# Performance work log

Hardware: AMD Instinct MI355X
Metric: run time of the kernel (lower is better)

Reference implementation:

```python
import jax, jax.numpy as jnp
import numpy as np
import math

D_MODEL = 1024
D_ATTN = 128
D_MID = 128
L = 4096

def setup_inputs() -> dict:
    key = jax.random.key(0)
    ks = jax.random.split(key, 5)
    scale = 1.0 / math.sqrt(D_MODEL)
    return {
        "x": jax.random.normal(ks[0], (L, D_MODEL), jnp.float32),
        "z": jax.random.normal(ks[1], (L, D_MODEL), jnp.float32),
        "Wq": jax.random.normal(ks[2], (D_MODEL, D_ATTN), jnp.float32) * scale,
        "bq": jnp.zeros((D_ATTN,), jnp.float32),
        "Wk": jax.random.normal(ks[3], (D_MODEL, D_ATTN), jnp.float32) * scale,
        "bk": jnp.zeros((D_ATTN,), jnp.float32),
        "Wv": jax.random.normal(ks[4], (D_MODEL, D_MID), jnp.float32) * scale,
        "bv": jnp.zeros((D_MID,), jnp.float32),
    }

def reference(x, z, Wq, bq, Wk, bk, Wv, bv):
    # q: [L_x, d_attn], k: [L_z, d_attn], v: [L_z, d_mid]
    q = x @ Wq + bq
    k = z @ Wk + bk
    v = z @ Wv + bv
    inv_sqrt_d = 1.0 / math.sqrt(D_ATTN)
    s = (q @ k.T) * inv_sqrt_d            # [L_x, L_z]
    y = jax.nn.softmax(s, axis=-1) @ v    # [L_x, d_mid]
    return y
```

## Files before the change

### kernel.cpp

```cpp
#include <hip/hip_runtime.h>
#include <hip/hip_bf16.h>

typedef __attribute__((ext_vector_type(8))) short short8;
typedef __attribute__((ext_vector_type(4))) float f32x4;
typedef __attribute__((ext_vector_type(8))) _Float16 half8;

#define L_SEQ 4096
#define DM    1024
#define DA    128
#define AZ    16

#define OFF_QB  786432
#define OFF_KF  1835008
#define OFF_VF  2883584
#define OFF_OA  4063232
#define OA_BYTES ((size_t)AZ * L_SEQ * DA * 2)

__device__ __forceinline__ short f2bf(float f) {
    union { float f; unsigned u; } v; v.f = f;
    unsigned u = v.u;
    u += 0x7FFFu + ((u >> 16) & 1u);
    return (short)(u >> 16);
}

__device__ __forceinline__ unsigned cvt_pk_bf16(float lo, float hi) {
    unsigned r;
    asm("v_cvt_pk_bf16_f32 %0, %1, %2" : "=v"(r) : "v"(lo), "v"(hi));
    return r;
}

typedef const __attribute__((address_space(1))) void g_void_t;
typedef __attribute__((address_space(3))) void l_void_t;
__device__ __forceinline__ void g2lds16(const void* g, void* l) {
    __builtin_amdgcn_global_load_lds((g_void_t*)g, (l_void_t*)l, 16, 0, 0);
}

__global__ __launch_bounds__(256) void prep_w_kernel(
    const float* __restrict__ Wq, const float* __restrict__ Wk,
    const float* __restrict__ Wv, short8* __restrict__ WTf)
{
    const int m = blockIdx.y, kidx = blockIdx.x;
    const float* __restrict__ W = (m == 0) ? Wq : (m == 1) ? Wk : Wv;
    __shared__ __align__(16) float Ws[32 * 132];
    const int t = threadIdx.x;
#pragma unroll
    for (int i = 0; i < 4; i++) {
        const int u = i * 256 + t;
        const int kk = u >> 5, n4 = (u & 31) * 4;
        *(f32x4*)&Ws[kk * 132 + n4] = *(const f32x4*)&W[(size_t)(kidx * 32 + kk) * DA + n4];
    }
    __syncthreads();
#pragma unroll
    for (int i = 0; i < 2; i++) {
        const int u = i * 256 + t;
        const int nt = u >> 6, lane = u & 63, l16 = lane & 15, quad = lane >> 4;
        short8 fr;
#pragma unroll
        for (int j = 0; j < 8; j++)
            fr[j] = f2bf(Ws[(quad * 8 + j) * 132 + nt * 16 + l16]);
        WTf[((size_t)(m * 32 + kidx) * 8 + nt) * 64 + lane] = fr;
    }
}

__global__ __launch_bounds__(256, 1) void qkv_kernel(
    const float* __restrict__ x, const float* __restrict__ z,
    const char* __restrict__ WTraw,
    const float* __restrict__ bq, const float* __restrict__ bk,
    const float* __restrict__ bv,
    short* __restrict__ qb, short8* __restrict__ kf, short8* __restrict__ vf)
{
    __shared__ __align__(16) char smem[2][32768];

    const int t = threadIdx.x;
    const int wave = t >> 6, lane = t & 63;
    const int l16 = lane & 15, quad = lane >> 4;
    const int mtile = wave >> 1, nhalf = wave & 1;
    const int isKV = blockIdx.y;
    const int m1 = isKV ? 1 : 0;
    const int row0 = blockIdx.x * 32;
    const int nbytes = isKV ? 32768 : 16384;

    const float* __restrict__ Am = isKV ? z : x;
    const float* ap = Am + (size_t)(row0 + mtile * 16 + l16) * DM + quad * 8;

    f32x4 acc1[4], acc2[4];
#pragma unroll
    for (int i = 0; i < 4; i++) {
        acc1[i] = (f32x4){0.f, 0.f, 0.f, 0.f};
        acc2[i] = (f32x4){0.f, 0.f, 0.f, 0.f};
    }

    auto stage = [&](int it2, int b) {
        const char* base1 = WTraw + (size_t)(m1 * 32 + it2 * 2) * 8192;
        const char* base2 = WTraw + (size_t)(2 * 32 + it2 * 2) * 8192;
#pragma unroll
        for (int i = 0; i < 8; i++) {
            const int off = i * 4096 + wave * 1024;
            if (off < nbytes) {
                const char* src = (off < 16384) ? (base1 + off) : (base2 + (off - 16384));
                g2lds16(src + lane * 16, &smem[b][off]);
            }
        }
    };

    f32x4 cur[4], nxt[4];
#pragma unroll
    for (int j = 0; j < 2; j++) {
        cur[j * 2]     = *(const f32x4*)(ap + j * 32);
        cur[j * 2 + 1] = *(const f32x4*)(ap + j * 32 + 4);
        nxt[j * 2]     = *(const f32x4*)(ap + 64 + j * 32);
        nxt[j * 2 + 1] = *(const f32x4*)(ap + 64 + j * 32 + 4);
    }

    stage(0, 0);
    __syncthreads();

#pragma unroll 1
    for (int it = 0; it < 16; it++) {
        const int b = it & 1;
        if (it + 1 < 16) stage(it + 1, b ^ 1);

        const int ipf = (it + 2 < 16) ? it + 2 : it;
        f32x4 fut[4];
#pragma unroll
        for (int j = 0; j < 2; j++) {
            fut[j * 2]     = *(const f32x4*)(ap + ipf * 64 + j * 32);
            fut[j * 2 + 1] = *(const f32x4*)(ap + ipf * 64 + j * 32 + 4);
        }

#pragma unroll
        for (int ss = 0; ss < 2; ss++) {
            short8 afr;
#pragma unroll
            for (int j = 0; j < 4; j++) {
                afr[j]     = f2bf(cur[ss * 2][j]);
                afr[4 + j] = f2bf(cur[ss * 2 + 1][j]);
            }
#pragma unroll
            for (int ntl = 0; ntl < 4; ntl++) {
                short8 bfr = *(const short8*)&smem[b][ss * 8192 + ((nhalf * 4 + ntl) * 64 + lane) * 16];
                acc1[ntl] = __builtin_amdgcn_mfma_f32_16x16x32_bf16(afr, bfr, acc1[ntl], 0, 0, 0);
            }
            if (isKV) {
#pragma unroll
                for (int ntl = 0; ntl < 4; ntl++) {
                    short8 bfr = *(const short8*)&smem[b][16384 + ss * 8192 + ((nhalf * 4 + ntl) * 64 + lane) * 16];
                    acc2[ntl] = __builtin_amdgcn_mfma_f32_16x16x32_bf16(afr, bfr, acc2[ntl], 0, 0, 0);
                }
            }
        }
        __syncthreads();
#pragma unroll
        for (int j = 0; j < 4; j++) { cur[j] = nxt[j]; nxt[j] = fut[j]; }
    }

    if (!isKV) {
        const float CL2E = 0.1275187669712930f;
#pragma unroll
        for (int ntl = 0; ntl < 4; ntl++) {
            const int col = nhalf * 64 + ntl * 16 + l16;
            const float bb = bq[col];
#pragma unroll
            for (int r = 0; r < 4; r++)
                qb[(size_t)(row0 + mtile * 16 + quad * 4 + r) * DA + col] =
                    f2bf((acc1[ntl][r] + bb) * CL2E);
        }
        return;
    }

    short* kT = (short*)&smem[0][0];
    short* vT = (short*)&smem[0][16384];
#pragma unroll
    for (int ntl = 0; ntl < 4; ntl++) {
        const int col = nhalf * 64 + ntl * 16 + l16;
        const float bbk = bk[col], bbv = bv[col];
#pragma unroll
        for (int r = 0; r < 4; r++) {
            const int rl = mtile * 16 + quad * 4 + r;
            kT[rl * 132 + col] = f2bf(acc1[ntl][r] + bbk);
            vT[rl * 132 + col] = f2bf(acc2[ntl][r] + bbv);
        }
    }
    __syncthreads();

    const int kg = blockIdx.x;
#pragma unroll
    for (int i = 0; i < 2; i++) {
        const int f = i * 256 + t;
        const int ks = f >> 7, nth = (f >> 6) & 1, ln = f & 63;
        const int lf = ln & 15, qf = ln >> 4;
        short8 fr;
#pragma unroll
        for (int j = 0; j < 8; j++)
            fr[j] = kT[(nth * 16 + lf) * 132 + ks * 32 + qf * 8 + j];
        kf[((size_t)(kg * 4 + ks) * 2 + nth) * 64 + ln] = fr;
    }
#pragma unroll
    for (int i = 0; i < 2; i++) {
        const int f = i * 256 + t;
        const int nt = f >> 6, ln = f & 63;
        const int lf = ln & 15, qf = ln >> 4;
        short8 fr;
#pragma unroll
        for (int j = 0; j < 8; j++)
            fr[j] = vT[(qf * 8 + j) * 132 + nt * 16 + lf];
        vf[((size_t)kg * 8 + nt) * 64 + ln] = fr;
    }
}

__global__ __launch_bounds__(256, 2) void attn_kernel(
    const short* __restrict__ qb, const char* __restrict__ kfg,
    const char* __restrict__ vfg, _Float16* __restrict__ OA,
    float* __restrict__ lA)
{
    __shared__ __align__(16) char kv[2][8192];

    const int t    = threadIdx.x;
    const int wave = t >> 6;
    const int lane = t & 63;
    const int l16  = lane & 15;
    const int quad = lane >> 4;
    const int qr0  = blockIdx.x * 128;
    const int g0   = blockIdx.y * 8;

    auto stage = [&](int g, int b) {
        const char* kb_ = kfg + (size_t)(g0 + g) * 8192 + wave * 2048;
        g2lds16(kb_ + lane * 16,        &kv[b][wave * 2048]);
        g2lds16(kb_ + 1024 + lane * 16, &kv[b][wave * 2048 + 1024]);
    };

    stage(0, 0);

    short8 af[2][4];
#pragma unroll
    for (int mt = 0; mt < 2; mt++) {
        const short* qrow = qb + (size_t)(qr0 + wave * 32 + mt * 16 + l16) * DA + quad * 8;
#pragma unroll
        for (int ks = 0; ks < 4; ks++)
            af[mt][ks] = *(const short8*)(qrow + ks * 32);
    }

    short8 bones;
#pragma unroll
    for (int j = 0; j < 8; j++) bones[j] = (l16 == 0) ? (short)0x3F80 : (short)0;

    f32x4 O[2][9];
#pragma unroll
    for (int mt = 0; mt < 2; mt++)
#pragma unroll
        for (int i = 0; i < 9; i++) O[mt][i] = (f32x4){0.f, 0.f, 0.f, 0.f};

    __syncthreads();

#pragma unroll 1
    for (int g = 0; g < 8; g++) {
        const int b = g & 1;
        if (g + 1 < 8) stage(g + 1, b ^ 1);

        const short8* vgp = (const short8*)(vfg + (size_t)(g0 + g) * 8192);
        short8 b2v[8];
#pragma unroll
        for (int nt = 0; nt < 8; nt++)
            b2v[nt] = vgp[nt * 64 + lane];

        const char* kb_ = &kv[b][0];

        f32x4 st[2][2];
#pragma unroll
        for (int zh = 0; zh < 2; zh++)
#pragma unroll
            for (int mt = 0; mt < 2; mt++) st[zh][mt] = (f32x4){0.f, 0.f, 0.f, 0.f};
#pragma unroll
        for (int ks = 0; ks < 4; ks++)
#pragma unroll
            for (int zh = 0; zh < 2; zh++) {
                const short8 kfr = *(const short8*)(kb_ + ((ks * 2 + zh) * 64 + lane) * 16);
                st[zh][0] = __builtin_amdgcn_mfma_f32_16x16x32_bf16(kfr, af[0][ks], st[zh][0], 0, 0, 0);
                st[zh][1] = __builtin_amdgcn_mfma_f32_16x16x32_bf16(kfr, af[1][ks], st[zh][1], 0, 0, 0);
            }

        short8 a2[2];
#pragma unroll
        for (int mt = 0; mt < 2; mt++) {
            unsigned x0 = cvt_pk_bf16(exp2f(st[0][mt][0]), exp2f(st[0][mt][1]));
            unsigned x1 = cvt_pk_bf16(exp2f(st[0][mt][2]), exp2f(st[0][mt][3]));
            unsigned y0 = cvt_pk_bf16(exp2f(st[1][mt][0]), exp2f(st[1][mt][1]));
            unsigned y1 = cvt_pk_bf16(exp2f(st[1][mt][2]), exp2f(st[1][mt][3]));
            asm volatile("v_permlane32_swap_b32 %0, %1" : "+v"(x0), "+v"(y0));
            asm volatile("v_permlane32_swap_b32 %0, %1" : "+v"(x1), "+v"(y1));
            asm volatile("v_permlane16_swap_b32 %0, %1" : "+v"(x0), "+v"(y0));
            asm volatile("v_permlane16_swap_b32 %0, %1" : "+v"(x1), "+v"(y1));
            union { short8 s; unsigned u[4]; } pa;
            pa.u[0] = x0;
            pa.u[1] = x1;
            pa.u[2] = y0;
            pa.u[3] = y1;
            a2[mt] = pa.s;
        }

#pragma unroll
        for (int nt = 0; nt < 8; nt++) {
            O[0][nt] = __builtin_amdgcn_mfma_f32_16x16x32_bf16(a2[0], b2v[nt], O[0][nt], 0, 0, 0);
            O[1][nt] = __builtin_amdgcn_mfma_f32_16x16x32_bf16(a2[1], b2v[nt], O[1][nt], 0, 0, 0);
        }
        O[0][8] = __builtin_amdgcn_mfma_f32_16x16x32_bf16(a2[0], bones, O[0][8], 0, 0, 0);
        O[1][8] = __builtin_amdgcn_mfma_f32_16x16x32_bf16(a2[1], bones, O[1][8], 0, 0, 0);
        __syncthreads();
    }

    const int rw = qr0 + wave * 32;
    _Float16* Ob = OA + (size_t)blockIdx.y * L_SEQ * DA;
#pragma unroll
    for (int mt = 0; mt < 2; mt++)
#pragma unroll
        for (int nt = 0; nt < 8; nt++)
#pragma unroll
            for (int r = 0; r < 4; r++)
                Ob[(size_t)(rw + mt * 16 + quad * 4 + r) * DA + nt * 16 + l16] =
                    (_Float16)O[mt][nt][r];
    if (l16 == 0) {
        float* lb = lA + (size_t)blockIdx.y * L_SEQ;
#pragma unroll
        for (int mt = 0; mt < 2; mt++)
#pragma unroll
            for (int r = 0; r < 4; r++)
                lb[rw + mt * 16 + quad * 4 + r] = O[mt][8][r];
    }
}

__global__ __launch_bounds__(256) void merge_kernel(
    const _Float16* __restrict__ OA, const float* __restrict__ lA,
    float* __restrict__ out)
{
    const int t = threadIdx.x;
    const int row = blockIdx.x * 16 + (t >> 4);
    const int cg = (t & 15) * 8;

    float acc[8];
#pragma unroll
    for (int j = 0; j < 8; j++) acc[j] = 0.f;
    float lsum = 0.f;
#pragma unroll
    for (int zz = 0; zz < AZ; zz++) {
        const half8 v = *(const half8*)&OA[((size_t)zz * L_SEQ + row) * DA + cg];
#pragma unroll
        for (int j = 0; j < 8; j++) acc[j] += (float)v[j];
        lsum += lA[(size_t)zz * L_SEQ + row];
    }
    const float inv = 1.f / lsum;
    f32x4 o0, o1;
#pragma unroll
    for (int j = 0; j < 4; j++) { o0[j] = acc[j] * inv; o1[j] = acc[4 + j] * inv; }
    f32x4* dst = (f32x4*)&out[(size_t)row * DA + cg];
    dst[0] = o0;
    dst[1] = o1;
}

extern "C" void kernel_launch(void* const* d_in, const int* in_sizes, int n_in,
                              void* d_out, int out_size, void* d_ws, size_t ws_size,
                              hipStream_t stream) {
    (void)in_sizes; (void)n_in; (void)out_size; (void)ws_size;
    const float* x  = (const float*)d_in[0];
    const float* z  = (const float*)d_in[1];
    const float* Wq = (const float*)d_in[2];
    const float* bq = (const float*)d_in[3];
    const float* Wk = (const float*)d_in[4];
    const float* bk = (const float*)d_in[5];
    const float* Wv = (const float*)d_in[6];
    const float* bv = (const float*)d_in[7];
    float* out = (float*)d_out;

    short8*   WTf = (short8*)d_ws;
    short*    qb  = (short*)((char*)d_ws + OFF_QB);
    short8*   kf  = (short8*)((char*)d_ws + OFF_KF);
    short8*   vf  = (short8*)((char*)d_ws + OFF_VF);
    _Float16* OA  = (_Float16*)((char*)d_ws + OFF_OA);
    float*    lA  = (float*)((char*)d_ws + OFF_OA + OA_BYTES);

    prep_w_kernel<<<dim3(32, 3), 256, 0, stream>>>(Wq, Wk, Wv, WTf);
    qkv_kernel<<<dim3(128, 2), 256, 0, stream>>>(x, z, (const char*)WTf,
                                                 bq, bk, bv, qb, kf, vf);
    attn_kernel<<<dim3(32, AZ), 256, 0, stream>>>(qb, (const char*)kf,
                                                  (const char*)vf, OA, lA);
    merge_kernel<<<256, 256, 0, stream>>>(OA, lA, out);
}
```

Before: 126.3 us.

## Fuse split-K merge into attention kernel via last-block atomic counter

```diff
diff --git a/kernel.cpp b/kernel.cpp
--- a/kernel.cpp
+++ b/kernel.cpp
@@ -15,6 +15,8 @@
 #define OFF_VF  2883584
 #define OFF_OA  4063232
 #define OA_BYTES ((size_t)AZ * L_SEQ * DA * 2)
+#define LA_BYTES ((size_t)AZ * L_SEQ * 4)
+#define OFF_CNT (OFF_OA + OA_BYTES + LA_BYTES)
 
 __device__ __forceinline__ short f2bf(float f) {
     union { float f; unsigned u; } v; v.f = f;
@@ -37,12 +39,14 @@
 
 __global__ __launch_bounds__(256) void prep_w_kernel(
     const float* __restrict__ Wq, const float* __restrict__ Wk,
-    const float* __restrict__ Wv, short8* __restrict__ WTf)
+    const float* __restrict__ Wv, short8* __restrict__ WTf,
+    int* __restrict__ cnt)
 {
     const int m = blockIdx.y, kidx = blockIdx.x;
+    const int t = threadIdx.x;
+    if (m == 0 && kidx == 0 && t < 32) cnt[t] = 0;
     const float* __restrict__ W = (m == 0) ? Wq : (m == 1) ? Wk : Wv;
     __shared__ __align__(16) float Ws[32 * 132];
-    const int t = threadIdx.x;
 #pragma unroll
     for (int i = 0; i < 4; i++) {
         const int u = i * 256 + t;
@@ -211,9 +215,10 @@
 __global__ __launch_bounds__(256, 2) void attn_kernel(
     const short* __restrict__ qb, const char* __restrict__ kfg,
     const char* __restrict__ vfg, _Float16* __restrict__ OA,
-    float* __restrict__ lA)
+    float* __restrict__ lA, int* __restrict__ cnt, float* __restrict__ out)
 {
     __shared__ __align__(16) char kv[2][8192];
+    __shared__ int isLast;
 
     const int t    = threadIdx.x;
     const int wave = t >> 6;
@@ -270,6 +275,7 @@
         for (int zh = 0; zh < 2; zh++)
 #pragma unroll
             for (int mt = 0; mt < 2; mt++) st[zh][mt] = (f32x4){0.f, 0.f, 0.f, 0.f};
+        __builtin_amdgcn_s_setprio(1);
 #pragma unroll
         for (int ks = 0; ks < 4; ks++)
 #pragma unroll
@@ -278,6 +284,7 @@
                 st[zh][0] = __builtin_amdgcn_mfma_f32_16x16x32_bf16(kfr, af[0][ks], st[zh][0], 0, 0, 0);
                 st[zh][1] = __builtin_amdgcn_mfma_f32_16x16x32_bf16(kfr, af[1][ks], st[zh][1], 0, 0, 0);
             }
+        __builtin_amdgcn_s_setprio(0);
 
         short8 a2[2];
 #pragma unroll
@@ -298,6 +305,7 @@
             a2[mt] = pa.s;
         }
 
+        __builtin_amdgcn_s_setprio(1);
 #pragma unroll
         for (int nt = 0; nt < 8; nt++) {
             O[0][nt] = __builtin_amdgcn_mfma_f32_16x16x32_bf16(a2[0], b2v[nt], O[0][nt], 0, 0, 0);
@@ -305,6 +313,7 @@
         }
         O[0][8] = __builtin_amdgcn_mfma_f32_16x16x32_bf16(a2[0], bones, O[0][8], 0, 0, 0);
         O[1][8] = __builtin_amdgcn_mfma_f32_16x16x32_bf16(a2[1], bones, O[1][8], 0, 0, 0);
+        __builtin_amdgcn_s_setprio(0);
         __syncthreads();
     }
 
@@ -326,34 +335,39 @@
             for (int r = 0; r < 4; r++)
                 lb[rw + mt * 16 + quad * 4 + r] = O[mt][8][r];
     }
-}
-
-__global__ __launch_bounds__(256) void merge_kernel(
-    const _Float16* __restrict__ OA, const float* __restrict__ lA,
-    float* __restrict__ out)
-{
-    const int t = threadIdx.x;
-    const int row = blockIdx.x * 16 + (t >> 4);
-    const int cg = (t & 15) * 8;
-
-    float acc[8];
-#pragma unroll
-    for (int j = 0; j < 8; j++) acc[j] = 0.f;
-    float lsum = 0.f;
-#pragma unroll
-    for (int zz = 0; zz < AZ; zz++) {
-        const half8 v = *(const half8*)&OA[((size_t)zz * L_SEQ + row) * DA + cg];
-#pragma unroll
-        for (int j = 0; j < 8; j++) acc[j] += (float)v[j];
-        lsum += lA[(size_t)zz * L_SEQ + row];
-    }
-    const float inv = 1.f / lsum;
-    f32x4 o0, o1;
-#pragma unroll
-    for (int j = 0; j < 4; j++) { o0[j] = acc[j] * inv; o1[j] = acc[4 + j] * inv; }
-    f32x4* dst = (f32x4*)&out[(size_t)row * DA + cg];
-    dst[0] = o0;
-    dst[1] = o1;
+
+    __threadfence();
+    __syncthreads();
+    if (t == 0)
+        isLast = (atomicAdd(&cnt[blockIdx.x], 1) == AZ - 1) ? 1 : 0;
+    __syncthreads();
+    if (isLast) {
+        __threadfence();
+        const int rowb = t >> 4;
+        const int cg   = (t & 15) * 8;
+#pragma unroll 1
+        for (int i = 0; i < 8; i++) {
+            const int row = qr0 + i * 16 + rowb;
+            float acc[8];
+#pragma unroll
+            for (int j = 0; j < 8; j++) acc[j] = 0.f;
+            float lsum = 0.f;
+#pragma unroll 1
+            for (int zz = 0; zz < AZ; zz++) {
+                const half8 v = *(const half8*)&OA[((size_t)zz * L_SEQ + row) * DA + cg];
+#pragma unroll
+                for (int j = 0; j < 8; j++) acc[j] += (float)v[j];
+                lsum += lA[(size_t)zz * L_SEQ + row];
+            }
+            const float inv = 1.f / lsum;
+            f32x4 o0, o1;
+#pragma unroll
+            for (int j = 0; j < 4; j++) { o0[j] = acc[j] * inv; o1[j] = acc[4 + j] * inv; }
+            f32x4* dst = (f32x4*)&out[(size_t)row * DA + cg];
+            dst[0] = o0;
+            dst[1] = o1;
+        }
+    }
 }
 
 extern "C" void kernel_launch(void* const* d_in, const int* in_sizes, int n_in,
@@ -376,11 +390,12 @@
     short8*   vf  = (short8*)((char*)d_ws + OFF_VF);
     _Float16* OA  = (_Float16*)((char*)d_ws + OFF_OA);
     float*    lA  = (float*)((char*)d_ws + OFF_OA + OA_BYTES);
-
-    prep_w_kernel<<<dim3(32, 3), 256, 0, stream>>>(Wq, Wk, Wv, WTf);
+    int*      cnt = (int*)((char*)d_ws + OFF_CNT);
+
+    prep_w_kernel<<<dim3(32, 3), 256, 0, stream>>>(Wq, Wk, Wv, WTf, cnt);
     qkv_kernel<<<dim3(128, 2), 256, 0, stream>>>(x, z, (const char*)WTf,
                                                  bq, bk, bv, qb, kf, vf);
     attn_kernel<<<dim3(32, AZ), 256, 0, stream>>>(qb, (const char*)kf,
-                                                  (const char*)vf, OA, lA);
-    merge_kernel<<<256, 256, 0, stream>>>(OA, lA, out);
-}
+                                                  (const char*)vf, OA, lA,
+                                                  cnt, out);
+}
```

Result: slower. 219.5 us (+73.8%).
